# Kernel optimization log

Measured on AMD Instinct MI355X. Metric: run time of the kernel, lower is better.

## Reference

```python
import jax, jax.numpy as jnp
import numpy as np

B, S, ENC, DEC, EMB, V = 256, 128, 512, 512, 256, 32000


def setup_inputs() -> dict:
    key = jax.random.key(0)
    ks = jax.random.split(key, 12)
    inp = {}
    inp["input_tok"] = jax.random.randint(ks[0], (B,), 0, V)
    inp["hidden"] = jax.random.normal(ks[1], (1, B, DEC), dtype=jnp.float32)
    inp["encoder_outputs"] = jax.random.normal(ks[2], (S, B, ENC), dtype=jnp.float32)
    # learned params
    inp["emb_table"] = jax.random.normal(ks[3], (V, EMB), dtype=jnp.float32) * 0.02
    inp["attn_W"] = jax.random.normal(ks[4], (ENC + DEC, DEC), dtype=jnp.float32) * 0.02
    inp["attn_b"] = jnp.zeros((DEC,), dtype=jnp.float32)
    inp["v"] = jax.random.uniform(ks[5], (DEC,), dtype=jnp.float32)
    inp["W_ih"] = jax.random.normal(ks[6], (3 * DEC, ENC + EMB), dtype=jnp.float32) * 0.02
    inp["W_hh"] = jax.random.normal(ks[7], (3 * DEC, DEC), dtype=jnp.float32) * 0.02
    inp["b_ih"] = jnp.zeros((3 * DEC,), dtype=jnp.float32)
    inp["b_hh"] = jnp.zeros((3 * DEC,), dtype=jnp.float32)
    inp["fc_W"] = jax.random.normal(ks[8], (V, ENC + DEC + EMB), dtype=jnp.float32) * 0.02
    inp["fc_b"] = jnp.zeros((V,), dtype=jnp.float32)
    return inp


def reference(input_tok, hidden, encoder_outputs, emb_table, attn_W, attn_b, v,
              W_ih, W_hh, b_ih, b_hh, fc_W, fc_b):
    # dropout is identity in eval mode
    emb = emb_table[input_tok]                      # [B, EMB]
    h = hidden[0]                                   # [B, DEC]
    s_len = encoder_outputs.shape[0]
    # Bahdanau attention: energy over [src_len, B]
    h_rep = jnp.broadcast_to(h[None], (s_len,) + h.shape)        # [S,B,DEC]
    cat = jnp.concatenate([h_rep, encoder_outputs], axis=-1)     # [S,B,ENC+DEC]
    energy = jnp.tanh(cat @ attn_W + attn_b)                     # [S,B,DEC]
    scores = jnp.einsum('sbd,d->bs', energy, v)                  # [B,S]
    a = jax.nn.softmax(scores, axis=1)                           # [B,S]
    weighted = jnp.einsum('bs,sbe->be', a, encoder_outputs)      # [B,ENC]
    # single-step GRU (PyTorch gate order: r, z, n)
    x = jnp.concatenate([emb, weighted], axis=1)                 # [B,EMB+ENC]
    gi = x @ W_ih.T + b_ih                                       # [B,3*DEC]
    gh = h @ W_hh.T + b_hh
    ir, iz, in_ = jnp.split(gi, 3, axis=1)
    hr, hz, hn = jnp.split(gh, 3, axis=1)
    r = jax.nn.sigmoid(ir + hr)
    z = jax.nn.sigmoid(iz + hz)
    n = jnp.tanh(in_ + r * hn)
    h_new = (1.0 - z) * n + z * h                                # [B,DEC]
    # output projection
    pred = jnp.concatenate([h_new, weighted, emb], axis=1) @ fc_W.T + fc_b  # [B,V]
    return pred, h_new
```

## Files before the change

### kernel.cpp

```cpp
#include <hip/hip_runtime.h>
#include <cmath>

static constexpr int B   = 256;
static constexpr int S   = 128;
static constexpr int ENC = 512;
static constexpr int DEC = 512;
static constexpr int EMB = 256;
static constexpr int V   = 32000;
static constexpr int KX  = EMB + ENC;
static constexpr int KF  = DEC + ENC + EMB;
static constexpr int G3  = 3 * DEC;

typedef __attribute__((ext_vector_type(8))) short short8v;
typedef __attribute__((ext_vector_type(4))) float f32x4;

__device__ __forceinline__ float sigmoidf(float xv) { return 1.0f / (1.0f + expf(-xv)); }

__device__ __forceinline__ unsigned short f2bf(float f) {
    unsigned u = __float_as_uint(f);
    unsigned r = (u + 0x7fffu + ((u >> 16) & 1u)) >> 16;
    return (unsigned short)r;
}

template<int TRANSB, int BIAS>
__global__ __launch_bounds__(256) void gemm_f32(
    const float* __restrict__ A, const float* __restrict__ Bm,
    const float* __restrict__ bias, float* __restrict__ C,
    int M, int N, int K, int lda, int ldb, int ldc)
{
    __shared__ float As[16][68];
    __shared__ float Bs[16][68];
    const int tid  = threadIdx.x;
    const int row0 = blockIdx.y * 64;
    const int col0 = blockIdx.x * 64;
    const int tx = tid & 15, ty = tid >> 4;

    float acc[4][4] = {};
    for (int k0 = 0; k0 < K; k0 += 16) {
        {
            const int m  = tid >> 2;
            const int kk = (tid & 3) << 2;
            const float4 a4 = *reinterpret_cast<const float4*>(
                &A[(size_t)(row0 + m) * lda + k0 + kk]);
            As[kk + 0][m] = a4.x; As[kk + 1][m] = a4.y;
            As[kk + 2][m] = a4.z; As[kk + 3][m] = a4.w;
        }
        if (TRANSB) {
            const int n  = tid >> 2;
            const int kk = (tid & 3) << 2;
            const float4 b4 = *reinterpret_cast<const float4*>(
                &Bm[(size_t)(col0 + n) * ldb + k0 + kk]);
            Bs[kk + 0][n] = b4.x; Bs[kk + 1][n] = b4.y;
            Bs[kk + 2][n] = b4.z; Bs[kk + 3][n] = b4.w;
        } else {
            const int kk = tid >> 4;
            const int n  = (tid & 15) << 2;
            *reinterpret_cast<float4*>(&Bs[kk][n]) =
                *reinterpret_cast<const float4*>(&Bm[(size_t)(k0 + kk) * ldb + col0 + n]);
        }
        __syncthreads();
        #pragma unroll
        for (int k = 0; k < 16; ++k) {
            float a4[4], b4[4];
            *reinterpret_cast<float4*>(a4) = *reinterpret_cast<const float4*>(&As[k][ty << 2]);
            *reinterpret_cast<float4*>(b4) = *reinterpret_cast<const float4*>(&Bs[k][tx << 2]);
            #pragma unroll
            for (int i = 0; i < 4; ++i)
                #pragma unroll
                for (int j = 0; j < 4; ++j)
                    acc[i][j] = fmaf(a4[i], b4[j], acc[i][j]);
        }
        __syncthreads();
    }
    #pragma unroll
    for (int i = 0; i < 4; ++i) {
        const int r = row0 + (ty << 2) + i;
        #pragma unroll
        for (int j = 0; j < 4; ++j) {
            const int c = col0 + (tx << 2) + j;
            float outv = acc[i][j];
            if (BIAS) outv += bias[c];
            C[(size_t)r * ldc + c] = outv;
        }
    }
}

__global__ __launch_bounds__(256) void transpose_We(
    const float* __restrict__ attn_W, unsigned short* __restrict__ WeT)
{
    __shared__ float t[32][33];
    const int k0 = blockIdx.x * 32, n0 = blockIdx.y * 32;
    const int r = threadIdx.x >> 3, c4 = (threadIdx.x & 7) * 4;
    const float4 f = *reinterpret_cast<const float4*>(
        &attn_W[(size_t)(DEC + k0 + r) * DEC + n0 + c4]);
    t[r][c4] = f.x; t[r][c4 + 1] = f.y; t[r][c4 + 2] = f.z; t[r][c4 + 3] = f.w;
    __syncthreads();
    unsigned short o[4] = { f2bf(t[c4 + 0][r]), f2bf(t[c4 + 1][r]),
                            f2bf(t[c4 + 2][r]), f2bf(t[c4 + 3][r]) };
    *reinterpret_cast<uint2*>(&WeT[(size_t)(n0 + r) * 512 + k0 + c4]) =
        *reinterpret_cast<uint2*>(o);
}

__global__ __launch_bounds__(512) void energy_mfma(
    const float* __restrict__ enc, const unsigned short* __restrict__ WeT,
    const float* __restrict__ hWb, const float* __restrict__ vvec,
    float* __restrict__ scores)
{
    __shared__ unsigned short Ae[256 * 40];
    __shared__ unsigned short Be[256 * 40];
    const int bid = blockIdx.x;
    const int logical = (bid & 7) * 32 + (bid >> 3);
    const int mb = logical >> 1, nb = logical & 1;
    const int tid = threadIdx.x, lane = tid & 63, wid = tid >> 6;
    const int wm = wid >> 2, wn = wid & 3;
    const int l15 = lane & 15, lk = lane >> 4;

    f32x4 acc[8][4] = {};
    for (int k0 = 0; k0 < 512; k0 += 32) {
        #pragma unroll
        for (int j = 0; j < 2; ++j) {
            const int ci = tid + 512 * j;
            const int row = ci >> 2, kc = ci & 3;
            const float* src = &enc[(size_t)(mb * 256 + row) * ENC + k0 + kc * 8];
            const float4 f0 = *reinterpret_cast<const float4*>(src);
            const float4 f1 = *reinterpret_cast<const float4*>(src + 4);
            short8v t;
            t[0] = (short)f2bf(f0.x); t[1] = (short)f2bf(f0.y);
            t[2] = (short)f2bf(f0.z); t[3] = (short)f2bf(f0.w);
            t[4] = (short)f2bf(f1.x); t[5] = (short)f2bf(f1.y);
            t[6] = (short)f2bf(f1.z); t[7] = (short)f2bf(f1.w);
            *reinterpret_cast<short8v*>(&Ae[row * 40 + kc * 8]) = t;
            *reinterpret_cast<short8v*>(&Be[row * 40 + kc * 8]) =
                *reinterpret_cast<const short8v*>(
                    &WeT[(size_t)(nb * 256 + row) * 512 + k0 + kc * 8]);
        }
        __syncthreads();
        short8v bfr[4];
        #pragma unroll
        for (int nf = 0; nf < 4; ++nf)
            bfr[nf] = *reinterpret_cast<const short8v*>(
                &Be[(wn * 64 + nf * 16 + l15) * 40 + lk * 8]);
        #pragma unroll
        for (int mf = 0; mf < 8; ++mf) {
            const short8v afr = *reinterpret_cast<const short8v*>(
                &Ae[(wm * 128 + mf * 16 + l15) * 40 + lk * 8]);
            #pragma unroll
            for (int nf = 0; nf < 4; ++nf)
                acc[mf][nf] = __builtin_amdgcn_mfma_f32_16x16x32_bf16(
                    afr, bfr[nf], acc[mf][nf], 0, 0, 0);
        }
        __syncthreads();
    }
    const int colbase = nb * 256 + wn * 64;
    #pragma unroll
    for (int mf = 0; mf < 8; ++mf) {
        const int rl0 = wm * 128 + mf * 16 + lk * 4;
        #pragma unroll
        for (int r = 0; r < 4; ++r) {
            const int rl = rl0 + r;
            float p = 0.0f;
            #pragma unroll
            for (int nf = 0; nf < 4; ++nf) {
                const int col = colbase + nf * 16 + l15;
                p += vvec[col] * tanhf(acc[mf][nf][r] + hWb[(size_t)rl * DEC + col]);
            }
            p += __shfl_xor(p, 1, 64);
            p += __shfl_xor(p, 2, 64);
            p += __shfl_xor(p, 4, 64);
            p += __shfl_xor(p, 8, 64);
            if (l15 == 0) atomicAdd(&scores[(size_t)mb * 256 + rl], p);
        }
    }
}

__global__ __launch_bounds__(256) void fc_mfma(
    const unsigned short* __restrict__ xcatb, const float* __restrict__ fcW,
    const float* __restrict__ fcb, float* __restrict__ pred)
{
    __shared__ unsigned short As[256 * 72];
    __shared__ unsigned short Bs[64 * 72];
    const int n0 = blockIdx.x * 64;
    const int tid = threadIdx.x, lane = tid & 63, wid = tid >> 6;
    const int wm = wid & 1, wn = wid >> 1;
    const int l15 = lane & 15, lk = lane >> 4;

    f32x4 acc[8][2] = {};
    for (int k0 = 0; k0 < KF; k0 += 64) {
        #pragma unroll
        for (int j = 0; j < 8; ++j) {
            const int ci = tid + 256 * j;
            const int row = ci >> 3, kc = ci & 7;
            *reinterpret_cast<short8v*>(&As[row * 72 + kc * 8]) =
                *reinterpret_cast<const short8v*>(
                    &xcatb[(size_t)row * KF + k0 + kc * 8]);
        }
        #pragma unroll
        for (int j = 0; j < 2; ++j) {
            const int ci = tid + 256 * j;
            const int row = ci >> 3, kc = ci & 7;
            const float* src = &fcW[(size_t)(n0 + row) * KF + k0 + kc * 8];
            const float4 f0 = *reinterpret_cast<const float4*>(src);
            const float4 f1 = *reinterpret_cast<const float4*>(src + 4);
            short8v t;
            t[0] = (short)f2bf(f0.x); t[1] = (short)f2bf(f0.y);
            t[2] = (short)f2bf(f0.z); t[3] = (short)f2bf(f0.w);
            t[4] = (short)f2bf(f1.x); t[5] = (short)f2bf(f1.y);
            t[6] = (short)f2bf(f1.z); t[7] = (short)f2bf(f1.w);
            *reinterpret_cast<short8v*>(&Bs[row * 72 + kc * 8]) = t;
        }
        __syncthreads();
        #pragma unroll
        for (int kk = 0; kk < 2; ++kk) {
            short8v bfr[2];
            #pragma unroll
            for (int nf = 0; nf < 2; ++nf)
                bfr[nf] = *reinterpret_cast<const short8v*>(
                    &Bs[(wn * 32 + nf * 16 + l15) * 72 + kk * 32 + lk * 8]);
            #pragma unroll
            for (int mf = 0; mf < 8; ++mf) {
                const short8v afr = *reinterpret_cast<const short8v*>(
                    &As[(wm * 128 + mf * 16 + l15) * 72 + kk * 32 + lk * 8]);
                acc[mf][0] = __builtin_amdgcn_mfma_f32_16x16x32_bf16(
                    afr, bfr[0], acc[mf][0], 0, 0, 0);
                acc[mf][1] = __builtin_amdgcn_mfma_f32_16x16x32_bf16(
                    afr, bfr[1], acc[mf][1], 0, 0, 0);
            }
        }
        __syncthreads();
    }
    #pragma unroll
    for (int mf = 0; mf < 8; ++mf) {
        const int grow0 = wm * 128 + mf * 16 + lk * 4;
        #pragma unroll
        for (int nf = 0; nf < 2; ++nf) {
            const int gcol = n0 + wn * 32 + nf * 16 + l15;
            const float bias = fcb[gcol];
            #pragma unroll
            for (int r = 0; r < 4; ++r)
                pred[(size_t)(grow0 + r) * V + gcol] = acc[mf][nf][r] + bias;
        }
    }
}

__global__ __launch_bounds__(256) void softmax_weighted(
    const float* __restrict__ scores, const float* __restrict__ enc,
    unsigned short* __restrict__ xcatb, float* __restrict__ x)
{
    const int b   = blockIdx.x;
    const int tid = threadIdx.x;
    __shared__ float sa[S];
    __shared__ float red[128];

    const float sc = (tid < S) ? scores[(size_t)tid * B + b] : -1e30f;
    if (tid < 128) red[tid] = sc;
    __syncthreads();
    for (int off = 64; off >= 1; off >>= 1) {
        if (tid < off) red[tid] = fmaxf(red[tid], red[tid + off]);
        __syncthreads();
    }
    const float mx = red[0];
    __syncthreads();
    const float e = (tid < S) ? expf(sc - mx) : 0.0f;
    if (tid < 128) red[tid] = e;
    __syncthreads();
    for (int off = 64; off >= 1; off >>= 1) {
        if (tid < off) red[tid] += red[tid + off];
        __syncthreads();
    }
    const float inv = 1.0f / red[0];
    __syncthreads();
    if (tid < S) sa[tid] = e * inv;
    __syncthreads();

    float acc0 = 0.0f, acc1 = 0.0f;
    const int e0 = tid * 2;
    for (int s = 0; s < S; ++s) {
        const float w = sa[s];
        const float2 v2 = *reinterpret_cast<const float2*>(
            &enc[((size_t)s * B + b) * ENC + e0]);
        acc0 = fmaf(w, v2.x, acc0);
        acc1 = fmaf(w, v2.y, acc1);
    }
    *reinterpret_cast<float2*>(&x[(size_t)b * KX + EMB + e0]) = make_float2(acc0, acc1);
    unsigned short t2[2] = { f2bf(acc0), f2bf(acc1) };
    *reinterpret_cast<unsigned int*>(&xcatb[(size_t)b * KF + DEC + e0]) =
        *reinterpret_cast<unsigned int*>(t2);
}

__global__ void gather_emb(const int* __restrict__ tok, const float* __restrict__ table,
                           unsigned short* __restrict__ xcatb, float* __restrict__ x)
{
    const int b = blockIdx.x, t = threadIdx.x;
    const float4 v4 = *reinterpret_cast<const float4*>(
        &table[(size_t)tok[b] * EMB + t * 4]);
    *reinterpret_cast<float4*>(&x[(size_t)b * KX + t * 4]) = v4;
    unsigned short o[4] = { f2bf(v4.x), f2bf(v4.y), f2bf(v4.z), f2bf(v4.w) };
    *reinterpret_cast<uint2*>(&xcatb[(size_t)b * KF + DEC + ENC + t * 4]) =
        *reinterpret_cast<uint2*>(o);
}

__global__ __launch_bounds__(256) void gru_gates(
    const float* __restrict__ gi, const float* __restrict__ gh,
    const float* __restrict__ h, unsigned short* __restrict__ xcatb,
    float* __restrict__ h_out)
{
    const int idx = blockIdx.x * 256 + threadIdx.x;
    const int b = idx >> 9, d = idx & 511;
    const float* gib = gi + (size_t)b * G3;
    const float* ghb = gh + (size_t)b * G3;
    const float r  = sigmoidf(gib[d] + ghb[d]);
    const float z  = sigmoidf(gib[DEC + d] + ghb[DEC + d]);
    const float n  = tanhf(gib[2 * DEC + d] + r * ghb[2 * DEC + d]);
    const float hv = h[(size_t)b * DEC + d];
    const float hn = (1.0f - z) * n + z * hv;
    xcatb[(size_t)b * KF + d] = f2bf(hn);
    h_out[(size_t)b * DEC + d] = hn;
}

extern "C" void kernel_launch(void* const* d_in, const int* in_sizes, int n_in,
                              void* d_out, int out_size, void* d_ws, size_t ws_size,
                              hipStream_t stream)
{
    const int*   tok    = (const int*)d_in[0];
    const float* hidden = (const float*)d_in[1];
    const float* enc    = (const float*)d_in[2];
    const float* table  = (const float*)d_in[3];
    const float* attn_W = (const float*)d_in[4];
    const float* attn_b = (const float*)d_in[5];
    const float* vvec   = (const float*)d_in[6];
    const float* W_ih   = (const float*)d_in[7];
    const float* W_hh   = (const float*)d_in[8];
    const float* b_ih   = (const float*)d_in[9];
    const float* b_hh   = (const float*)d_in[10];
    const float* fc_W   = (const float*)d_in[11];
    const float* fc_b   = (const float*)d_in[12];

    float* ws     = (float*)d_ws;
    float* hWb    = ws;
    float* scores = hWb + B * DEC;
    float* x      = scores + S * B;
    float* gi     = x + B * KX;
    float* gh     = gi + B * G3;
    unsigned short* xcatb = (unsigned short*)(gh + B * G3);
    unsigned short* WeT   = xcatb + (size_t)B * KF;

    float* pred  = (float*)d_out;
    float* h_out = pred + (size_t)B * V;

    hipMemsetAsync(scores, 0, (size_t)S * B * sizeof(float), stream);

    transpose_We<<<dim3(16, 16), 256, 0, stream>>>(attn_W, WeT);
    gather_emb<<<B, 64, 0, stream>>>(tok, table, xcatb, x);

    gemm_f32<0, 1><<<dim3(DEC / 64, B / 64), 256, 0, stream>>>(
        hidden, attn_W, attn_b, hWb, B, DEC, DEC, DEC, DEC, DEC);

    energy_mfma<<<256, 512, 0, stream>>>(enc, WeT, hWb, vvec, scores);

    softmax_weighted<<<B, 256, 0, stream>>>(scores, enc, xcatb, x);

    gemm_f32<1, 1><<<dim3(G3 / 64, B / 64), 256, 0, stream>>>(
        x, W_ih, b_ih, gi, B, G3, KX, KX, KX, G3);
    gemm_f32<1, 1><<<dim3(G3 / 64, B / 64), 256, 0, stream>>>(
        hidden, W_hh, b_hh, gh, B, G3, DEC, DEC, DEC, G3);

    gru_gates<<<(B * DEC) / 256, 256, 0, stream>>>(gi, gh, hidden, xcatb, h_out);

    fc_mfma<<<V / 64, 256, 0, stream>>>(xcatb, fc_W, fc_b, pred);
}
```

Before: 526.9 us.

## Pre-convert encoder and hidden to bf16, retile energy and fc, MFMA GRU gemms

Adds kernels that convert encoder_outputs and hidden to bf16 once, so the energy GEMM and the softmax-weighted sum read half the bytes and do no in-loop conversion. The energy kernel is retiled to 128-row M tiles with K=64 steps over 512 blocks, and the fc kernel moves to 128-column tiles with 512 threads. The GRU input and hidden GEMMs switch from fp32 SIMT to a bf16 MFMA kernel. The extra conversion pass adds a full read and write of the encoder tensor, and bf16 inputs to the GRU GEMMs lower precision.

```diff
diff --git a/kernel.cpp b/kernel.cpp
--- a/kernel.cpp
+++ b/kernel.cpp
@@ -20,6 +20,9 @@
     unsigned u = __float_as_uint(f);
     unsigned r = (u + 0x7fffu + ((u >> 16) & 1u)) >> 16;
     return (unsigned short)r;
+}
+__device__ __forceinline__ float bf2f(unsigned short s) {
+    return __uint_as_float(((unsigned)s) << 16);
 }
 
 template<int TRANSB, int BIAS>
@@ -85,6 +88,38 @@
     }
 }
 
+__global__ __launch_bounds__(256) void conv_enc(
+    const float* __restrict__ src, unsigned short* __restrict__ dst)
+{
+    size_t base = ((size_t)blockIdx.x * 256 + threadIdx.x) * 8;
+    const size_t stride = (size_t)2048 * 256 * 8;
+    #pragma unroll
+    for (int it = 0; it < 4; ++it, base += stride) {
+        const float4 f0 = *reinterpret_cast<const float4*>(&src[base]);
+        const float4 f1 = *reinterpret_cast<const float4*>(&src[base + 4]);
+        short8v t;
+        t[0] = (short)f2bf(f0.x); t[1] = (short)f2bf(f0.y);
+        t[2] = (short)f2bf(f0.z); t[3] = (short)f2bf(f0.w);
+        t[4] = (short)f2bf(f1.x); t[5] = (short)f2bf(f1.y);
+        t[6] = (short)f2bf(f1.z); t[7] = (short)f2bf(f1.w);
+        *reinterpret_cast<short8v*>(&dst[base]) = t;
+    }
+}
+
+__global__ __launch_bounds__(256) void conv_h(
+    const float* __restrict__ src, unsigned short* __restrict__ dst)
+{
+    const size_t base = ((size_t)blockIdx.x * 256 + threadIdx.x) * 8;
+    const float4 f0 = *reinterpret_cast<const float4*>(&src[base]);
+    const float4 f1 = *reinterpret_cast<const float4*>(&src[base + 4]);
+    short8v t;
+    t[0] = (short)f2bf(f0.x); t[1] = (short)f2bf(f0.y);
+    t[2] = (short)f2bf(f0.z); t[3] = (short)f2bf(f0.w);
+    t[4] = (short)f2bf(f1.x); t[5] = (short)f2bf(f1.y);
+    t[6] = (short)f2bf(f1.z); t[7] = (short)f2bf(f1.w);
+    *reinterpret_cast<short8v*>(&dst[base]) = t;
+}
+
 __global__ __launch_bounds__(256) void transpose_We(
     const float* __restrict__ attn_W, unsigned short* __restrict__ WeT)
 {
@@ -101,94 +136,97 @@
         *reinterpret_cast<uint2*>(o);
 }
 
-__global__ __launch_bounds__(512) void energy_mfma(
-    const float* __restrict__ enc, const unsigned short* __restrict__ WeT,
+__global__ __launch_bounds__(512, 4) void energy_mfma(
+    const unsigned short* __restrict__ encb, const unsigned short* __restrict__ WeT,
     const float* __restrict__ hWb, const float* __restrict__ vvec,
     float* __restrict__ scores)
 {
-    __shared__ unsigned short Ae[256 * 40];
-    __shared__ unsigned short Be[256 * 40];
+    __shared__ unsigned short Ae[128 * 72];
+    __shared__ unsigned short Be[256 * 72];
     const int bid = blockIdx.x;
-    const int logical = (bid & 7) * 32 + (bid >> 3);
+    const int logical = (bid & 7) * 64 + (bid >> 3);
     const int mb = logical >> 1, nb = logical & 1;
     const int tid = threadIdx.x, lane = tid & 63, wid = tid >> 6;
     const int wm = wid >> 2, wn = wid & 3;
     const int l15 = lane & 15, lk = lane >> 4;
 
-    f32x4 acc[8][4] = {};
-    for (int k0 = 0; k0 < 512; k0 += 32) {
+    f32x4 acc[4][4] = {};
+    for (int k0 = 0; k0 < 512; k0 += 64) {
         #pragma unroll
         for (int j = 0; j < 2; ++j) {
             const int ci = tid + 512 * j;
-            const int row = ci >> 2, kc = ci & 3;
-            const float* src = &enc[(size_t)(mb * 256 + row) * ENC + k0 + kc * 8];
-            const float4 f0 = *reinterpret_cast<const float4*>(src);
-            const float4 f1 = *reinterpret_cast<const float4*>(src + 4);
-            short8v t;
-            t[0] = (short)f2bf(f0.x); t[1] = (short)f2bf(f0.y);
-            t[2] = (short)f2bf(f0.z); t[3] = (short)f2bf(f0.w);
-            t[4] = (short)f2bf(f1.x); t[5] = (short)f2bf(f1.y);
-            t[6] = (short)f2bf(f1.z); t[7] = (short)f2bf(f1.w);
-            *reinterpret_cast<short8v*>(&Ae[row * 40 + kc * 8]) = t;
-            *reinterpret_cast<short8v*>(&Be[row * 40 + kc * 8]) =
+            const int row = ci >> 3, kc = ci & 7;
+            *reinterpret_cast<short8v*>(&Ae[row * 72 + kc * 8]) =
+                *reinterpret_cast<const short8v*>(
+                    &encb[(size_t)(mb * 128 + row) * 512 + k0 + kc * 8]);
+        }
+        #pragma unroll
+        for (int j = 0; j < 4; ++j) {
+            const int ci = tid + 512 * j;
+            const int row = ci >> 3, kc = ci & 7;
+            *reinterpret_cast<short8v*>(&Be[row * 72 + kc * 8]) =
                 *reinterpret_cast<const short8v*>(
                     &WeT[(size_t)(nb * 256 + row) * 512 + k0 + kc * 8]);
         }
         __syncthreads();
-        short8v bfr[4];
-        #pragma unroll
-        for (int nf = 0; nf < 4; ++nf)
-            bfr[nf] = *reinterpret_cast<const short8v*>(
-                &Be[(wn * 64 + nf * 16 + l15) * 40 + lk * 8]);
-        #pragma unroll
-        for (int mf = 0; mf < 8; ++mf) {
-            const short8v afr = *reinterpret_cast<const short8v*>(
-                &Ae[(wm * 128 + mf * 16 + l15) * 40 + lk * 8]);
+        #pragma unroll
+        for (int kk = 0; kk < 2; ++kk) {
+            short8v bfr[4];
             #pragma unroll
             for (int nf = 0; nf < 4; ++nf)
-                acc[mf][nf] = __builtin_amdgcn_mfma_f32_16x16x32_bf16(
-                    afr, bfr[nf], acc[mf][nf], 0, 0, 0);
+                bfr[nf] = *reinterpret_cast<const short8v*>(
+                    &Be[(wn * 64 + nf * 16 + l15) * 72 + kk * 32 + lk * 8]);
+            #pragma unroll
+            for (int mf = 0; mf < 4; ++mf) {
+                const short8v afr = *reinterpret_cast<const short8v*>(
+                    &Ae[(wm * 64 + mf * 16 + l15) * 72 + kk * 32 + lk * 8]);
+                #pragma unroll
+                for (int nf = 0; nf < 4; ++nf)
+                    acc[mf][nf] = __builtin_amdgcn_mfma_f32_16x16x32_bf16(
+                        afr, bfr[nf], acc[mf][nf], 0, 0, 0);
+            }
         }
         __syncthreads();
     }
     const int colbase = nb * 256 + wn * 64;
     #pragma unroll
-    for (int mf = 0; mf < 8; ++mf) {
-        const int rl0 = wm * 128 + mf * 16 + lk * 4;
+    for (int mf = 0; mf < 4; ++mf) {
         #pragma unroll
         for (int r = 0; r < 4; ++r) {
-            const int rl = rl0 + r;
+            const int rl = wm * 64 + mf * 16 + lk * 4 + r;
+            const int g  = mb * 128 + rl;
+            const int b  = g & (B - 1);
             float p = 0.0f;
             #pragma unroll
             for (int nf = 0; nf < 4; ++nf) {
                 const int col = colbase + nf * 16 + l15;
-                p += vvec[col] * tanhf(acc[mf][nf][r] + hWb[(size_t)rl * DEC + col]);
+                p += vvec[col] * tanhf(acc[mf][nf][r] + hWb[(size_t)b * DEC + col]);
             }
             p += __shfl_xor(p, 1, 64);
             p += __shfl_xor(p, 2, 64);
             p += __shfl_xor(p, 4, 64);
             p += __shfl_xor(p, 8, 64);
-            if (l15 == 0) atomicAdd(&scores[(size_t)mb * 256 + rl], p);
-        }
-    }
-}
-
-__global__ __launch_bounds__(256) void fc_mfma(
+            if (l15 == 0) atomicAdd(&scores[g], p);
+        }
+    }
+}
+
+__global__ __launch_bounds__(512) void fc_mfma(
     const unsigned short* __restrict__ xcatb, const float* __restrict__ fcW,
     const float* __restrict__ fcb, float* __restrict__ pred)
 {
     __shared__ unsigned short As[256 * 72];
-    __shared__ unsigned short Bs[64 * 72];
-    const int n0 = blockIdx.x * 64;
+    __shared__ unsigned short Bs[128 * 72];
+    const int n0 = blockIdx.x * 128;
     const int tid = threadIdx.x, lane = tid & 63, wid = tid >> 6;
-    const int wm = wid & 1, wn = wid >> 1;
+    const int wm = wid >> 2, wn = wid & 3;
     const int l15 = lane & 15, lk = lane >> 4;
 
     f32x4 acc[8][2] = {};
     for (int k0 = 0; k0 < KF; k0 += 64) {
         #pragma unroll
-        for (int j = 0; j < 8; ++j) {
-            const int ci = tid + 256 * j;
+        for (int j = 0; j < 4; ++j) {
+            const int ci = tid + 512 * j;
             const int row = ci >> 3, kc = ci & 7;
             *reinterpret_cast<short8v*>(&As[row * 72 + kc * 8]) =
                 *reinterpret_cast<const short8v*>(
@@ -196,7 +234,7 @@
         }
         #pragma unroll
         for (int j = 0; j < 2; ++j) {
-            const int ci = tid + 256 * j;
+            const int ci = tid + 512 * j;
             const int row = ci >> 3, kc = ci & 7;
             const float* src = &fcW[(size_t)(n0 + row) * KF + k0 + kc * 8];
             const float4 f0 = *reinterpret_cast<const float4*>(src);
@@ -242,9 +280,78 @@
     }
 }
 
+__global__ __launch_bounds__(256) void gemm_bf16_small(
+    const unsigned short* __restrict__ Abf, const float* __restrict__ Wf,
+    const float* __restrict__ bias, float* __restrict__ C, int K, int ldc)
+{
+    __shared__ unsigned short As[256 * 72];
+    __shared__ unsigned short Bs[64 * 72];
+    const int n0 = blockIdx.x * 64;
+    const int tid = threadIdx.x, lane = tid & 63, wid = tid >> 6;
+    const int wm = wid >> 1, wn = wid & 1;
+    const int l15 = lane & 15, lk = lane >> 4;
+
+    f32x4 acc[8][2] = {};
+    for (int k0 = 0; k0 < K; k0 += 64) {
+        #pragma unroll
+        for (int j = 0; j < 8; ++j) {
+            const int ci = tid + 256 * j;
+            const int row = ci >> 3, kc = ci & 7;
+            *reinterpret_cast<short8v*>(&As[row * 72 + kc * 8]) =
+                *reinterpret_cast<const short8v*>(
+                    &Abf[(size_t)row * K + k0 + kc * 8]);
+        }
+        #pragma unroll
+        for (int j = 0; j < 2; ++j) {
+            const int ci = tid + 256 * j;
+            const int row = ci >> 3, kc = ci & 7;
+            const float* src = &Wf[(size_t)(n0 + row) * K + k0 + kc * 8];
+            const float4 f0 = *reinterpret_cast<const float4*>(src);
+            const float4 f1 = *reinterpret_cast<const float4*>(src + 4);
+            short8v t;
+            t[0] = (short)f2bf(f0.x); t[1] = (short)f2bf(f0.y);
+            t[2] = (short)f2bf(f0.z); t[3] = (short)f2bf(f0.w);
+            t[4] = (short)f2bf(f1.x); t[5] = (short)f2bf(f1.y);
+            t[6] = (short)f2bf(f1.z); t[7] = (short)f2bf(f1.w);
+            *reinterpret_cast<short8v*>(&Bs[row * 72 + kc * 8]) = t;
+        }
+        __syncthreads();
+        #pragma unroll
+        for (int kk = 0; kk < 2; ++kk) {
+            short8v bfr[2];
+            #pragma unroll
+            for (int nf = 0; nf < 2; ++nf)
+                bfr[nf] = *reinterpret_cast<const short8v*>(
+                    &Bs[(wn * 32 + nf * 16 + l15) * 72 + kk * 32 + lk * 8]);
+            #pragma unroll
+            for (int mf = 0; mf < 8; ++mf) {
+                const short8v afr = *reinterpret_cast<const short8v*>(
+                    &As[(wm * 128 + mf * 16 + l15) * 72 + kk * 32 + lk * 8]);
+                acc[mf][0] = __builtin_amdgcn_mfma_f32_16x16x32_bf16(
+                    afr, bfr[0], acc[mf][0], 0, 0, 0);
+                acc[mf][1] = __builtin_amdgcn_mfma_f32_16x16x32_bf16(
+                    afr, bfr[1], acc[mf][1], 0, 0, 0);
+            }
+        }
+        __syncthreads();
+    }
+    #pragma unroll
+    for (int mf = 0; mf < 8; ++mf) {
+        const int grow0 = wm * 128 + mf * 16 + lk * 4;
+        #pragma unroll
+        for (int nf = 0; nf < 2; ++nf) {
+            const int gcol = n0 + wn * 32 + nf * 16 + l15;
+            const float bv = bias[gcol];
+            #pragma unroll
+            for (int r = 0; r < 4; ++r)
+                C[(size_t)(grow0 + r) * ldc + gcol] = acc[mf][nf][r] + bv;
+        }
+    }
+}
+
 __global__ __launch_bounds__(256) void softmax_weighted(
-    const float* __restrict__ scores, const float* __restrict__ enc,
-    unsigned short* __restrict__ xcatb, float* __restrict__ x)
+    const float* __restrict__ scores, const unsigned short* __restrict__ encb,
+    unsigned short* __restrict__ xcatb, unsigned short* __restrict__ xb)
 {
     const int b   = blockIdx.x;
     const int tid = threadIdx.x;
@@ -276,27 +383,27 @@
     const int e0 = tid * 2;
     for (int s = 0; s < S; ++s) {
         const float w = sa[s];
-        const float2 v2 = *reinterpret_cast<const float2*>(
-            &enc[((size_t)s * B + b) * ENC + e0]);
-        acc0 = fmaf(w, v2.x, acc0);
-        acc1 = fmaf(w, v2.y, acc1);
-    }
-    *reinterpret_cast<float2*>(&x[(size_t)b * KX + EMB + e0]) = make_float2(acc0, acc1);
+        const unsigned u = *reinterpret_cast<const unsigned*>(
+            &encb[((size_t)s * B + b) * ENC + e0]);
+        acc0 = fmaf(w, bf2f((unsigned short)(u & 0xffffu)), acc0);
+        acc1 = fmaf(w, bf2f((unsigned short)(u >> 16)), acc1);
+    }
     unsigned short t2[2] = { f2bf(acc0), f2bf(acc1) };
-    *reinterpret_cast<unsigned int*>(&xcatb[(size_t)b * KF + DEC + e0]) =
-        *reinterpret_cast<unsigned int*>(t2);
+    const unsigned packed = *reinterpret_cast<unsigned*>(t2);
+    *reinterpret_cast<unsigned*>(&xcatb[(size_t)b * KF + DEC + e0]) = packed;
+    *reinterpret_cast<unsigned*>(&xb[(size_t)b * KX + EMB + e0])    = packed;
 }
 
 __global__ void gather_emb(const int* __restrict__ tok, const float* __restrict__ table,
-                           unsigned short* __restrict__ xcatb, float* __restrict__ x)
+                           unsigned short* __restrict__ xcatb, unsigned short* __restrict__ xb)
 {
     const int b = blockIdx.x, t = threadIdx.x;
     const float4 v4 = *reinterpret_cast<const float4*>(
         &table[(size_t)tok[b] * EMB + t * 4]);
-    *reinterpret_cast<float4*>(&x[(size_t)b * KX + t * 4]) = v4;
     unsigned short o[4] = { f2bf(v4.x), f2bf(v4.y), f2bf(v4.z), f2bf(v4.w) };
-    *reinterpret_cast<uint2*>(&xcatb[(size_t)b * KF + DEC + ENC + t * 4]) =
-        *reinterpret_cast<uint2*>(o);
+    const uint2 p = *reinterpret_cast<uint2*>(o);
+    *reinterpret_cast<uint2*>(&xcatb[(size_t)b * KF + DEC + ENC + t * 4]) = p;
+    *reinterpret_cast<uint2*>(&xb[(size_t)b * KX + t * 4]) = p;
 }
 
 __global__ __launch_bounds__(256) void gru_gates(
@@ -338,33 +445,35 @@
     float* ws     = (float*)d_ws;
     float* hWb    = ws;
     float* scores = hWb + B * DEC;
-    float* x      = scores + S * B;
-    float* gi     = x + B * KX;
+    float* gi     = scores + S * B;
     float* gh     = gi + B * G3;
     unsigned short* xcatb = (unsigned short*)(gh + B * G3);
     unsigned short* WeT   = xcatb + (size_t)B * KF;
+    unsigned short* xb    = WeT + (size_t)512 * 512;
+    unsigned short* hb    = xb + (size_t)B * KX;
+    unsigned short* encb  = hb + (size_t)B * DEC;
 
     float* pred  = (float*)d_out;
     float* h_out = pred + (size_t)B * V;
 
     hipMemsetAsync(scores, 0, (size_t)S * B * sizeof(float), stream);
 
+    conv_enc<<<2048, 256, 0, stream>>>(enc, encb);
+    conv_h<<<64, 256, 0, stream>>>(hidden, hb);
     transpose_We<<<dim3(16, 16), 256, 0, stream>>>(attn_W, WeT);
-    gather_emb<<<B, 64, 0, stream>>>(tok, table, xcatb, x);
+    gather_emb<<<B, 64, 0, stream>>>(tok, table, xcatb, xb);
 
     gemm_f32<0, 1><<<dim3(DEC / 64, B / 64), 256, 0, stream>>>(
         hidden, attn_W, attn_b, hWb, B, DEC, DEC, DEC, DEC, DEC);
 
-    energy_mfma<<<256, 512, 0, stream>>>(enc, WeT, hWb, vvec, scores);
-
-    softmax_weighted<<<B, 256, 0, stream>>>(scores, enc, xcatb, x);
-
-    gemm_f32<1, 1><<<dim3(G3 / 64, B / 64), 256, 0, stream>>>(
-        x, W_ih, b_ih, gi, B, G3, KX, KX, KX, G3);
-    gemm_f32<1, 1><<<dim3(G3 / 64, B / 64), 256, 0, stream>>>(
-        hidden, W_hh, b_hh, gh, B, G3, DEC, DEC, DEC, G3);
+    energy_mfma<<<512, 512, 0, stream>>>(encb, WeT, hWb, vvec, scores);
+
+    softmax_weighted<<<B, 256, 0, stream>>>(scores, encb, xcatb, xb);
+
+    gemm_bf16_small<<<G3 / 64, 256, 0, stream>>>(xb, W_ih, b_ih, gi, KX, G3);
+    gemm_bf16_small<<<G3 / 64, 256, 0, stream>>>(hb, W_hh, b_hh, gh, DEC, G3);
 
     gru_gates<<<(B * DEC) / 256, 256, 0, stream>>>(gi, gh, hidden, xcatb, h_out);
 
-    fc_mfma<<<V / 64, 256, 0, stream>>>(xcatb, fc_W, fc_b, pred);
-}
+    fc_mfma<<<V / 128, 512, 0, stream>>>(xcatb, fc_W, fc_b, pred);
+}
```

Result: faster. 490.6 us (-6.9%).
